# Performance work log

Hardware: AMD Instinct MI355X
Metric: run time of the kernel (lower is better)

Reference implementation:

```python
import jax, jax.numpy as jnp
import numpy as np

NEG_SLOPE_ATT = 0.2   # GATv2Conv attention leaky_relu slope
NEG_SLOPE_ACT = 0.01  # F.leaky_relu default between layers


def gatv2_layer(x, src, dst, edge_attr, Wl, Wr, We, att, concat):
    """PyG GATv2Conv (bias=False, residual=False, share_weights=False,
    add_self_loops=True with fill_value='mean' for edge_attr, eval mode)."""
    N = x.shape[0]
    H, C = att.shape
    E = src.shape[0]
    # self-loop edge attrs: mean of incoming edge attrs per node (fill_value='mean')
    deg = jax.ops.segment_sum(jnp.ones((E,), x.dtype), dst, num_segments=N)
    loop_attr = jax.ops.segment_sum(edge_attr, dst, num_segments=N) / jnp.maximum(deg, 1.0)[:, None]
    loop = jnp.arange(N)
    s = jnp.concatenate([src, loop])
    d = jnp.concatenate([dst, loop])
    ea = jnp.concatenate([edge_attr, loop_attr], axis=0)
    xl = (x @ Wl).reshape(N, H, C)  # lin_l -> source features (messages)
    xr = (x @ Wr).reshape(N, H, C)  # lin_r -> target features
    # edge-wise attention input: x_l[j] + x_r[i] + lin_edge(e_ij)  -> [E+N, H, C]
    e = xl[s] + xr[d] + (ea @ We).reshape(-1, H, C)
    e = jax.nn.leaky_relu(e, NEG_SLOPE_ATT)
    logits = jnp.einsum('ehc,hc->eh', e, att)  # [E+N, H]
    # numerically stable segment softmax over incoming edges per destination
    lmax = jax.ops.segment_max(logits, d, num_segments=N)  # every node has a self loop -> finite
    ex = jnp.exp(logits - lmax[d])
    denom = jax.ops.segment_sum(ex, d, num_segments=N)
    alpha = ex / (denom[d] + 1e-16)
    out = jax.ops.segment_sum(alpha[:, :, None] * xl[s], d, num_segments=N)  # [N, H, C]
    return out.reshape(N, H * C) if concat else out.mean(axis=1)


def setup_inputs() -> dict:
    key = jax.random.key(0)
    ks = jax.random.split(key, 12)
    N, E, F, H, C, EDIM, NCLS = 50000, 800000, 128, 4, 32, 16, 1
    HC = H * C  # 128
    sc = 0.1
    return {
        'x': jax.random.normal(ks[0], (N, F), jnp.float32),
        'edge_index': jax.random.randint(ks[1], (2, E), 0, N),
        'edge_attr': jax.random.normal(ks[2], (E, EDIM), jnp.float32),
        'Wl1': jax.random.normal(ks[3], (F, HC), jnp.float32) * sc,
        'Wr1': jax.random.normal(ks[4], (F, HC), jnp.float32) * sc,
        'We1': jax.random.normal(ks[5], (EDIM, HC), jnp.float32) * sc,
        'att1': jax.random.normal(ks[6], (H, C), jnp.float32) * sc,
        'Wl2': jax.random.normal(ks[7], (HC, H * NCLS), jnp.float32) * sc,
        'Wr2': jax.random.normal(ks[8], (HC, H * NCLS), jnp.float32) * sc,
        'We2': jax.random.normal(ks[9], (EDIM, H * NCLS), jnp.float32) * sc,
        'att2': jax.random.normal(ks[10], (H, NCLS), jnp.float32) * sc,
    }


def reference(x, edge_index, edge_attr, Wl1, Wr1, We1, att1, Wl2, Wr2, We2, att2):
    src, dst = edge_index[0], edge_index[1]
    h = gatv2_layer(x, src, dst, edge_attr, Wl1, Wr1, We1, att1, concat=True)
    h = jax.nn.leaky_relu(h, NEG_SLOPE_ACT)
    out = gatv2_layer(h, src, dst, edge_attr, Wl2, Wr2, We2, att2, concat=False)
    return out.reshape(-1)
```

## Files before the change

kernel.cpp:

```cpp
#include <hip/hip_runtime.h>
#include <math.h>


typedef __attribute__((ext_vector_type(8))) short bf16x8;
typedef __attribute__((ext_vector_type(4))) float f32x4;
typedef __attribute__((ext_vector_type(2))) float f32x2;
typedef _Float16 f16;
typedef __attribute__((ext_vector_type(2))) _Float16 f16x2;
typedef __attribute__((ext_vector_type(8))) _Float16 f16x8;

static __device__ __forceinline__ ushort f2bf(float f) {
    unsigned u = __float_as_uint(f);
    unsigned r = (u + 0x7fffu + ((u >> 16) & 1u)) >> 16;
    return (ushort)r;
}

static __device__ __forceinline__ float row_sum16(float x) {
    x += __int_as_float(__builtin_amdgcn_update_dpp(0, __float_as_int(x), 0x121, 0xf, 0xf, true));
    x += __int_as_float(__builtin_amdgcn_update_dpp(0, __float_as_int(x), 0x122, 0xf, 0xf, true));
    x += __int_as_float(__builtin_amdgcn_update_dpp(0, __float_as_int(x), 0x124, 0xf, 0xf, true));
    x += __int_as_float(__builtin_amdgcn_update_dpp(0, __float_as_int(x), 0x128, 0xf, 0xf, true));
    return x;
}

static __device__ __forceinline__ float red64(float x) {
    x = row_sum16(x);
    x += __shfl_xor(x, 16);
    x += __shfl_xor(x, 32);
    return x;
}

__global__ void k_count_deg(const int* __restrict__ dst, int* __restrict__ deg,
                            int* __restrict__ rank, int E) {
    int i = blockIdx.x * blockDim.x + threadIdx.x;
    if (i < E) rank[i] = atomicAdd(&deg[dst[i]], 1);
}

__global__ __launch_bounds__(1024) void k_scan1(const int* __restrict__ deg,
                                                int* __restrict__ rowptr,
                                                int* __restrict__ part, int N) {
    __shared__ int wsum[16];
    int t = threadIdx.x, l = t & 63, w = t >> 6;
    int i = blockIdx.x * 1024 + t;
    int v = (i < N) ? deg[i] : 0;
    int sc = v;
    #pragma unroll
    for (int off = 1; off < 64; off <<= 1) {
        int y = __shfl_up(sc, off);
        if (l >= off) sc += y;
    }
    if (l == 63) wsum[w] = sc;
    __syncthreads();
    if (w == 0) {
        int pv = (l < 16) ? wsum[l] : 0;
        int psc = pv;
        #pragma unroll
        for (int off = 1; off < 16; off <<= 1) {
            int y = __shfl_up(psc, off);
            if (l >= off) psc += y;
        }
        if (l < 16) wsum[l] = psc - pv;
    }
    __syncthreads();
    if (i < N) rowptr[i] = wsum[w] + sc - v;
    if (t == 1023) part[blockIdx.x] = wsum[15] + sc;
}

__global__ void k_scan2(int* __restrict__ part, int nb) {
    int l = threadIdx.x & 63;
    int run = 0;
    for (int base = 0; base < nb; base += 64) {
        int i = base + l;
        int v = (i < nb) ? part[i] : 0;
        int sc = v;
        #pragma unroll
        for (int off = 1; off < 64; off <<= 1) {
            int y = __shfl_up(sc, off);
            if (l >= off) sc += y;
        }
        if (i < nb) part[i] = run + sc - v;
        run += __shfl(sc, 63);
    }
}

__global__ void k_scan3(int* __restrict__ rowptr, const int* __restrict__ part, int N, int E) {
    int i = blockIdx.x * 256 + threadIdx.x;
    if (i < N) rowptr[i] += part[i >> 10];
    if (i == 0) rowptr[N] = E;
}

__global__ __launch_bounds__(256) void k_scatter_e(
    const int* __restrict__ dst, const int* __restrict__ src,
    const float* __restrict__ ea, const float* __restrict__ We2,
    const int* __restrict__ rowptr, const int* __restrict__ rank,
    f16* __restrict__ ea_f16, float* __restrict__ qe2,
    int* __restrict__ src_perm, int E) {
    __shared__ float sW[64];
    int t = threadIdx.x;
    if (t < 64) sW[t] = We2[t];
    __syncthreads();
    int i = blockIdx.x * 256 + t;
    if (i >= E) return;
    int d = dst[i];
    int pos = rowptr[d] + rank[i];
    src_perm[pos] = src[i];
    const float4* s4 = (const float4*)(ea + (size_t)i * 16);
    float4 r0 = s4[0], r1 = s4[1], r2 = s4[2], r3 = s4[3];
    f16x8 h0, h1;
    h0[0] = (f16)r0.x; h0[1] = (f16)r0.y; h0[2] = (f16)r0.z; h0[3] = (f16)r0.w;
    h0[4] = (f16)r1.x; h0[5] = (f16)r1.y; h0[6] = (f16)r1.z; h0[7] = (f16)r1.w;
    h1[0] = (f16)r2.x; h1[1] = (f16)r2.y; h1[2] = (f16)r2.z; h1[3] = (f16)r2.w;
    h1[4] = (f16)r3.x; h1[5] = (f16)r3.y; h1[6] = (f16)r3.z; h1[7] = (f16)r3.w;
    *(f16x8*)(ea_f16 + (size_t)pos * 16) = h0;
    *(f16x8*)(ea_f16 + (size_t)pos * 16 + 8) = h1;
    float a[16] = {r0.x, r0.y, r0.z, r0.w, r1.x, r1.y, r1.z, r1.w,
                   r2.x, r2.y, r2.z, r2.w, r3.x, r3.y, r3.z, r3.w};
    float q0 = 0.f, q1 = 0.f, q2v = 0.f, q3 = 0.f;
    #pragma unroll
    for (int k = 0; k < 16; ++k) {
        q0 += a[k] * sW[k * 4 + 0];
        q1 += a[k] * sW[k * 4 + 1];
        q2v += a[k] * sW[k * 4 + 2];
        q3 += a[k] * sW[k * 4 + 3];
    }
    *(float4*)(qe2 + (size_t)pos * 4) = make_float4(q0, q1, q2v, q3);
}

__global__ void k_wcvt(const float* __restrict__ Wl, const float* __restrict__ Wr,
                       const float* __restrict__ We1,
                       ushort* __restrict__ wcat_t, f16* __restrict__ we1h) {
    int i = blockIdx.x * 256 + threadIdx.x;
    if (i < 16 * 128) we1h[i] = (f16)We1[i];
    if (i >= 128 * 256) return;
    int n = i >> 7, k = i & 127;
    float v = (n < 128) ? Wl[k * 128 + n] : Wr[k * 128 + (n - 128)];
    wcat_t[i] = f2bf(v);
}

__global__ __launch_bounds__(256) void k_gemm1_mfma(
    const float* __restrict__ x, const ushort* __restrict__ wcat_t,
    ushort* __restrict__ xl, float* __restrict__ xr, int N) {
    __shared__ ushort xs[64 * 128];
    int t = threadIdx.x, l = t & 63, w = t >> 6;
    int r0 = blockIdx.x * 64;
    bf16x8 bf[4][4];
    {
        int coln = w * 64 + (l & 15);
        int kr = (l >> 4) * 8;
        #pragma unroll
        for (int nt = 0; nt < 4; ++nt)
            #pragma unroll
            for (int ks = 0; ks < 4; ++ks)
                bf[nt][ks] = *(const bf16x8*)&wcat_t[(size_t)(nt * 16 + coln) * 128 + ks * 32 + kr];
    }
    #pragma unroll
    for (int it = 0; it < 4; ++it) {
        int slot = t + 256 * it;
        int row = slot >> 4, ch = slot & 15;
        int grow = r0 + row;
        float v0 = 0.f, v1 = 0.f, v2 = 0.f, v3 = 0.f, v4 = 0.f, v5 = 0.f, v6 = 0.f, v7 = 0.f;
        if (grow < N) {
            float4 a = *(const float4*)(x + (size_t)grow * 128 + ch * 8);
            float4 b = *(const float4*)(x + (size_t)grow * 128 + ch * 8 + 4);
            v0 = a.x; v1 = a.y; v2 = a.z; v3 = a.w;
            v4 = b.x; v5 = b.y; v6 = b.z; v7 = b.w;
        }
        bf16x8 tv;
        tv[0] = (short)f2bf(v0); tv[1] = (short)f2bf(v1);
        tv[2] = (short)f2bf(v2); tv[3] = (short)f2bf(v3);
        tv[4] = (short)f2bf(v4); tv[5] = (short)f2bf(v5);
        tv[6] = (short)f2bf(v6); tv[7] = (short)f2bf(v7);
        int ch2 = ch ^ (row & 15);
        *(bf16x8*)&xs[row * 128 + ch2 * 8] = tv;
    }
    __syncthreads();
    f32x4 acc[4][4];
    #pragma unroll
    for (int mt = 0; mt < 4; ++mt)
        #pragma unroll
        for (int nt = 0; nt < 4; ++nt)
            acc[mt][nt] = (f32x4){0.f, 0.f, 0.f, 0.f};
    #pragma unroll
    for (int ks = 0; ks < 4; ++ks) {
        bf16x8 af[4];
        #pragma unroll
        for (int mt = 0; mt < 4; ++mt) {
            int row = mt * 16 + (l & 15);
            int ch = (ks * 4 + (l >> 4)) ^ (row & 15);
            af[mt] = *(const bf16x8*)&xs[row * 128 + ch * 8];
        }
        #pragma unroll
        for (int mt = 0; mt < 4; ++mt)
            #pragma unroll
            for (int nt = 0; nt < 4; ++nt)
                acc[mt][nt] = __builtin_amdgcn_mfma_f32_16x16x32_bf16(
                    af[mt], bf[nt][ks], acc[mt][nt], 0, 0, 0);
    }
    #pragma unroll
    for (int mt = 0; mt < 4; ++mt) {
        #pragma unroll
        for (int nt = 0; nt < 4; ++nt) {
            int colg = w * 64 + nt * 16 + (l & 15);
            #pragma unroll
            for (int r = 0; r < 4; ++r) {
                int rowg = r0 + mt * 16 + (l >> 4) * 4 + r;
                if (rowg < N) {
                    float val = acc[mt][nt][r];
                    if (colg < 128) xl[(size_t)rowg * 128 + colg] = f2bf(val);
                    else            xr[(size_t)rowg * 128 + (colg - 128)] = val;
                }
            }
        }
    }
}

__global__ __launch_bounds__(256, 4) void k_fused1_dot(
    const int* __restrict__ rowptr, const int* __restrict__ src_perm,
    const ushort* __restrict__ xl_bf, const float* __restrict__ xr,
    const f16* __restrict__ ea_f16, const f16* __restrict__ we1h,
    const float* __restrict__ att,
    const float* __restrict__ Wl2, const float* __restrict__ Wr2,
    float* __restrict__ xl2, float* __restrict__ xr2, int N) {
    int t = threadIdx.x, l = t & 63;
    int n = (blockIdx.x * 256 + t) >> 6;
    if (n >= N) return;
    const float RLN2 = 1.44269504f;
    const unsigned* xlw = (const unsigned*)xl_bf;
    f16x2 weX[8], weY[8];
    #pragma unroll
    for (int kp = 0; kp < 8; ++kp) {
        weX[kp][0] = we1h[(2 * kp) * 128 + 2 * l];
        weX[kp][1] = we1h[(2 * kp + 1) * 128 + 2 * l];
        weY[kp][0] = we1h[(2 * kp) * 128 + 2 * l + 1];
        weY[kp][1] = we1h[(2 * kp + 1) * 128 + 2 * l + 1];
    }
    f32x2 av = *(const f32x2*)(att + 2 * l);
    av = av * RLN2;
    f32x2 xrv = *(const f32x2*)(xr + (size_t)n * 128 + 2 * l);
    int rs = rowptr[n], re = rowptr[n + 1];
    int deg = re - rs;
    int urs = __builtin_amdgcn_readfirstlane(rs);
    f32x2 acc = {0.f, 0.f}, mq = {0.f, 0.f};
    float den = 0.f;
    #pragma unroll 2
    for (int slot = 0; slot < deg; ++slot) {
        unsigned jj = (unsigned)(urs + slot);
        const f16x2* ap = (const f16x2*)(ea_f16 + (size_t)jj * 16);
        int s = src_perm[jj];
        unsigned xw = xlw[(unsigned)s * 64u + (unsigned)l];
        float qx = 0.f, qy = 0.f;
        #pragma unroll
        for (int kp = 0; kp < 8; ++kp) {
            f16x2 a = ap[kp];
            qx = __builtin_amdgcn_fdot2(a, weX[kp], qx, false);
            qy = __builtin_amdgcn_fdot2(a, weY[kp], qy, false);
        }
        f32x2 q = {qx, qy};
        f32x2 xlv;
        xlv.x = __uint_as_float(xw << 16);
        xlv.y = __uint_as_float(xw & 0xffff0000u);
        f32x2 v = xrv + q + xlv;
        f32x2 u = __builtin_elementwise_max(v, 0.2f * v);
        f32x2 pt = av * u;
        float p = row_sum16(pt.x + pt.y);
        float w = exp2f(p);
        acc += xlv * w;
        den += w;
        mq += q;
    }
    {
        float inv = 1.f / (float)(deg > 1 ? deg : 1);
        f32x2 q = mq * inv;
        unsigned xw = xlw[(unsigned)n * 64u + (unsigned)l];
        f32x2 xlv;
        xlv.x = __uint_as_float(xw << 16);
        xlv.y = __uint_as_float(xw & 0xffff0000u);
        f32x2 v = xrv + q + xlv;
        f32x2 u = __builtin_elementwise_max(v, 0.2f * v);
        f32x2 pt = av * u;
        float p = row_sum16(pt.x + pt.y);
        float w = exp2f(p);
        acc += xlv * w;
        den += w;
    }
    float rdn = 1.f / (den + 1e-16f);
    float h0 = acc.x * rdn, h1 = acc.y * rdn;
    h0 = h0 > 0.f ? h0 : 0.01f * h0;
    h1 = h1 > 0.f ? h1 : 0.01f * h1;
    float4 wla = *(const float4*)(Wl2 + (size_t)(2 * l) * 4);
    float4 wlb = *(const float4*)(Wl2 + (size_t)(2 * l + 1) * 4);
    float4 wra = *(const float4*)(Wr2 + (size_t)(2 * l) * 4);
    float4 wrb = *(const float4*)(Wr2 + (size_t)(2 * l + 1) * 4);
    float q0 = red64(h0 * wla.x + h1 * wlb.x);
    float q1 = red64(h0 * wla.y + h1 * wlb.y);
    float q2 = red64(h0 * wla.z + h1 * wlb.z);
    float q3 = red64(h0 * wla.w + h1 * wlb.w);
    float q4 = red64(h0 * wra.x + h1 * wrb.x);
    float q5 = red64(h0 * wra.y + h1 * wrb.y);
    float q6 = red64(h0 * wra.z + h1 * wrb.z);
    float q7 = red64(h0 * wra.w + h1 * wrb.w);
    if (l == 0) {
        *(float4*)(xl2 + (size_t)n * 4) = make_float4(q0, q1, q2, q3);
        *(float4*)(xr2 + (size_t)n * 4) = make_float4(q4, q5, q6, q7);
    }
}

__global__ __launch_bounds__(256, 4) void k_fused2_q(
    const int* __restrict__ rowptr, const int* __restrict__ src_perm,
    const float* __restrict__ xl2, const float* __restrict__ xr2,
    const float* __restrict__ qe2, const float* __restrict__ att2,
    float* __restrict__ out, int N) {
    int t = threadIdx.x, l = t & 63, g = l & 15;
    int node = (((blockIdx.x * 256 + t) >> 6) << 2) + (l >> 4);
    if (node >= N) return;
    int rs = rowptr[node], re = rowptr[node + 1];
    int deg = re - rs;
    float4 xrv = *(const float4*)(xr2 + (size_t)node * 4);
    const float RLN2 = 1.44269504f;
    float a0 = att2[0] * RLN2, a1 = att2[1] * RLN2;
    float a2 = att2[2] * RLN2, a3 = att2[3] * RLN2;
    float ac0 = 0.f, ac1 = 0.f, ac2 = 0.f, ac3 = 0.f;
    float dn0 = 0.f, dn1 = 0.f, dn2 = 0.f, dn3 = 0.f;
    float mq0 = 0.f, mq1 = 0.f, mq2 = 0.f, mq3 = 0.f;
    for (int slot = g; slot < deg; slot += 16) {
        int row = rs + slot;
        int s = src_perm[row];
        float4 q = *(const float4*)(qe2 + (size_t)row * 4);
        float4 xv = *(const float4*)(xl2 + (size_t)s * 4);
        float v0 = xv.x + xrv.x + q.x; v0 = fmaxf(v0, 0.2f * v0);
        float v1 = xv.y + xrv.y + q.y; v1 = fmaxf(v1, 0.2f * v1);
        float v2 = xv.z + xrv.z + q.z; v2 = fmaxf(v2, 0.2f * v2);
        float v3 = xv.w + xrv.w + q.w; v3 = fmaxf(v3, 0.2f * v3);
        float w0 = exp2f(v0 * a0); ac0 += w0 * xv.x; dn0 += w0;
        float w1 = exp2f(v1 * a1); ac1 += w1 * xv.y; dn1 += w1;
        float w2 = exp2f(v2 * a2); ac2 += w2 * xv.z; dn2 += w2;
        float w3 = exp2f(v3 * a3); ac3 += w3 * xv.w; dn3 += w3;
        mq0 += q.x; mq1 += q.y; mq2 += q.z; mq3 += q.w;
    }
    ac0 = row_sum16(ac0); ac1 = row_sum16(ac1);
    ac2 = row_sum16(ac2); ac3 = row_sum16(ac3);
    dn0 = row_sum16(dn0); dn1 = row_sum16(dn1);
    dn2 = row_sum16(dn2); dn3 = row_sum16(dn3);
    mq0 = row_sum16(mq0); mq1 = row_sum16(mq1);
    mq2 = row_sum16(mq2); mq3 = row_sum16(mq3);
    {
        float inv = 1.f / (float)(deg > 1 ? deg : 1);
        float4 xv = *(const float4*)(xl2 + (size_t)node * 4);
        float v0 = xv.x + xrv.x + mq0 * inv; v0 = fmaxf(v0, 0.2f * v0);
        float v1 = xv.y + xrv.y + mq1 * inv; v1 = fmaxf(v1, 0.2f * v1);
        float v2 = xv.z + xrv.z + mq2 * inv; v2 = fmaxf(v2, 0.2f * v2);
        float v3 = xv.w + xrv.w + mq3 * inv; v3 = fmaxf(v3, 0.2f * v3);
        float w0 = exp2f(v0 * a0); ac0 += w0 * xv.x; dn0 += w0;
        float w1 = exp2f(v1 * a1); ac1 += w1 * xv.y; dn1 += w1;
        float w2 = exp2f(v2 * a2); ac2 += w2 * xv.z; dn2 += w2;
        float w3 = exp2f(v3 * a3); ac3 += w3 * xv.w; dn3 += w3;
    }
    if (g == 0) {
        float r = ac0 / (dn0 + 1e-16f) + ac1 / (dn1 + 1e-16f)
                + ac2 / (dn2 + 1e-16f) + ac3 / (dn3 + 1e-16f);
        out[node] = r * 0.25f;
    }
}

extern "C" void kernel_launch(void* const* d_in, const int* in_sizes, int n_in,
                              void* d_out, int out_size, void* d_ws, size_t ws_size,
                              hipStream_t stream) {
    const float* x         = (const float*)d_in[0];
    const int*   edge_index= (const int*)d_in[1];
    const float* edge_attr = (const float*)d_in[2];
    const float* Wl1       = (const float*)d_in[3];
    const float* Wr1       = (const float*)d_in[4];
    const float* We1       = (const float*)d_in[5];
    const float* att1      = (const float*)d_in[6];
    const float* Wl2       = (const float*)d_in[7];
    const float* Wr2       = (const float*)d_in[8];
    const float* We2       = (const float*)d_in[9];
    const float* att2      = (const float*)d_in[10];
    float* outp = (float*)d_out;

    const int F = 128, HC = 128;
    int N = in_sizes[0] / F;
    int E = in_sizes[1] / 2;
    const int* src = edge_index;
    const int* dst = edge_index + E;

    char* ws = (char*)d_ws;
    size_t off = 0;
    auto alloc = [&](size_t bytes) {
        char* p = ws + off;
        off += (bytes + 255) & ~(size_t)255;
        return p;
    };
    int*      deg      = (int*)alloc((size_t)N * 4);
    int*      rowptr   = (int*)alloc((size_t)(N + 1) * 4);
    int*      part     = (int*)alloc(((size_t)N / 1024 + 2) * 4);
    int*      rank     = (int*)alloc((size_t)E * 4);
    ushort*   wcat_t   = (ushort*)alloc((size_t)128 * 256 * 2);
    f16*      we1h     = (f16*)alloc((size_t)16 * 128 * 2);
    ushort*   xl_bf    = (ushort*)alloc((size_t)N * HC * 2);
    float*    xr1      = (float*)alloc((size_t)N * HC * 4);
    float*    xl2      = (float*)alloc((size_t)N * 4 * 4);
    float*    xr2      = (float*)alloc((size_t)N * 4 * 4);
    int*      src_perm = (int*)alloc((size_t)E * 4);
    float*    qe2      = (float*)alloc((size_t)E * 4 * 4);
    f16*      ea_f16   = (f16*)alloc((size_t)E * 16 * 2);

    int eb = (E + 255) / 256;
    int nb = (N + 1023) / 1024;

    hipMemsetAsync(deg, 0, (size_t)N * 4, stream);
    k_count_deg<<<eb, 256, 0, stream>>>(dst, deg, rank, E);
    k_scan1<<<nb, 1024, 0, stream>>>(deg, rowptr, part, N);
    k_scan2<<<1, 64, 0, stream>>>(part, nb);
    k_scan3<<<(N + 255) / 256, 256, 0, stream>>>(rowptr, part, N, E);
    k_scatter_e<<<eb, 256, 0, stream>>>(dst, src, edge_attr, We2, rowptr, rank,
                                        ea_f16, qe2, src_perm, E);
    k_wcvt<<<128, 256, 0, stream>>>(Wl1, Wr1, We1, wcat_t, we1h);
    k_gemm1_mfma<<<(N + 63) / 64, 256, 0, stream>>>(x, wcat_t, xl_bf, xr1, N);
    k_fused1_dot<<<(N + 3) / 4, 256, 0, stream>>>(rowptr, src_perm, xl_bf, xr1, ea_f16,
                                                  we1h, att1, Wl2, Wr2, xl2, xr2, N);
    k_fused2_q<<<(N + 15) / 16, 256, 0, stream>>>(rowptr, src_perm, xl2, xr2, qe2,
                                                  att2, outp, N);
}
```

Baseline: 214.6 us.

## Split wavefront into two half-waves processing two edges per iteration with prefetch

The layer-1 fused aggregation kernel now has each 64-lane wavefront handle two edges at once, with each 32-lane half owning 4 channels per lane. The head reduction shrinks to 8 lanes via DPP, and the two halves are combined with a cross-half shuffle at the end. The next edge's src index and xl row are software-prefetched, which aims to cut the serial per-edge latency chain of the gather loop. The cost is more registers (32 f16x2 weight registers, and the launch_bounds occupancy hint is removed) and masked wasted work when the degree is odd.

```diff
diff --git a/kernel.cpp b/kernel.cpp
--- a/kernel.cpp
+++ b/kernel.cpp
@@ -23,10 +23,10 @@
     return x;
 }
 
-static __device__ __forceinline__ float red64(float x) {
-    x = row_sum16(x);
-    x += __shfl_xor(x, 16);
-    x += __shfl_xor(x, 32);
+static __device__ __forceinline__ float sum8(float x) {
+    x += __int_as_float(__builtin_amdgcn_update_dpp(0, __float_as_int(x), 0xB1, 0xf, 0xf, true));
+    x += __int_as_float(__builtin_amdgcn_update_dpp(0, __float_as_int(x), 0x4E, 0xf, 0xf, true));
+    x += __int_as_float(__builtin_amdgcn_update_dpp(0, __float_as_int(x), 0x141, 0xf, 0xf, true));
     return x;
 }
 
@@ -214,7 +214,7 @@
     }
 }
 
-__global__ __launch_bounds__(256, 4) void k_fused1_dot(
+__global__ __launch_bounds__(256) void k_fused1_hw(
     const int* __restrict__ rowptr, const int* __restrict__ src_perm,
     const ushort* __restrict__ xl_bf, const float* __restrict__ xr,
     const f16* __restrict__ ea_f16, const f16* __restrict__ we1h,
@@ -222,83 +222,138 @@
     const float* __restrict__ Wl2, const float* __restrict__ Wr2,
     float* __restrict__ xl2, float* __restrict__ xr2, int N) {
     int t = threadIdx.x, l = t & 63;
+    int j = l & 31, half = l >> 5;
     int n = (blockIdx.x * 256 + t) >> 6;
     if (n >= N) return;
     const float RLN2 = 1.44269504f;
     const unsigned* xlw = (const unsigned*)xl_bf;
-    f16x2 weX[8], weY[8];
-    #pragma unroll
-    for (int kp = 0; kp < 8; ++kp) {
-        weX[kp][0] = we1h[(2 * kp) * 128 + 2 * l];
-        weX[kp][1] = we1h[(2 * kp + 1) * 128 + 2 * l];
-        weY[kp][0] = we1h[(2 * kp) * 128 + 2 * l + 1];
-        weY[kp][1] = we1h[(2 * kp + 1) * 128 + 2 * l + 1];
-    }
-    f32x2 av = *(const f32x2*)(att + 2 * l);
-    av = av * RLN2;
-    f32x2 xrv = *(const f32x2*)(xr + (size_t)n * 128 + 2 * l);
+    f16x2 w16[4][8];
+    #pragma unroll
+    for (int c = 0; c < 4; ++c)
+        #pragma unroll
+        for (int kp = 0; kp < 8; ++kp) {
+            w16[c][kp][0] = we1h[(2 * kp) * 128 + 4 * j + c];
+            w16[c][kp][1] = we1h[(2 * kp + 1) * 128 + 4 * j + c];
+        }
+    float4 av = *(const float4*)(att + 4 * j);
+    av.x *= RLN2; av.y *= RLN2; av.z *= RLN2; av.w *= RLN2;
+    float4 xrv = *(const float4*)(xr + (size_t)n * 128 + 4 * j);
     int rs = rowptr[n], re = rowptr[n + 1];
     int deg = re - rs;
     int urs = __builtin_amdgcn_readfirstlane(rs);
-    f32x2 acc = {0.f, 0.f}, mq = {0.f, 0.f};
+    float acc0 = 0.f, acc1 = 0.f, acc2 = 0.f, acc3 = 0.f;
+    float mq0 = 0.f, mq1 = 0.f, mq2 = 0.f, mq3 = 0.f;
     float den = 0.f;
-    #pragma unroll 2
-    for (int slot = 0; slot < deg; ++slot) {
-        unsigned jj = (unsigned)(urs + slot);
+    int niter = (deg + 1) >> 1;
+    float mk_nxt = 0.f;
+    unsigned jj_nxt = 0;
+    uint2 xw_nxt = make_uint2(0u, 0u);
+    if (niter > 0) {
+        int sA = half;
+        mk_nxt = (sA < deg) ? 1.f : 0.f;
+        int sc = (sA < deg) ? sA : (deg - 1);
+        jj_nxt = (unsigned)(urs + sc);
+        int s0 = src_perm[jj_nxt];
+        xw_nxt = *(const uint2*)(xlw + (size_t)(unsigned)s0 * 64u + 2u * j);
+    }
+    for (int it = 0; it < niter; ++it) {
+        float mk = mk_nxt;
+        unsigned jj = jj_nxt;
+        uint2 xw = xw_nxt;
+        if (it + 1 < niter) {
+            int sA = 2 * (it + 1) + half;
+            mk_nxt = (sA < deg) ? 1.f : 0.f;
+            int sc = (sA < deg) ? sA : (deg - 1);
+            jj_nxt = (unsigned)(urs + sc);
+            int s1 = src_perm[jj_nxt];
+            xw_nxt = *(const uint2*)(xlw + (size_t)(unsigned)s1 * 64u + 2u * j);
+        }
         const f16x2* ap = (const f16x2*)(ea_f16 + (size_t)jj * 16);
-        int s = src_perm[jj];
-        unsigned xw = xlw[(unsigned)s * 64u + (unsigned)l];
-        float qx = 0.f, qy = 0.f;
+        float q0 = 0.f, q1 = 0.f, q2 = 0.f, q3 = 0.f;
         #pragma unroll
         for (int kp = 0; kp < 8; ++kp) {
             f16x2 a = ap[kp];
-            qx = __builtin_amdgcn_fdot2(a, weX[kp], qx, false);
-            qy = __builtin_amdgcn_fdot2(a, weY[kp], qy, false);
-        }
-        f32x2 q = {qx, qy};
-        f32x2 xlv;
-        xlv.x = __uint_as_float(xw << 16);
-        xlv.y = __uint_as_float(xw & 0xffff0000u);
-        f32x2 v = xrv + q + xlv;
-        f32x2 u = __builtin_elementwise_max(v, 0.2f * v);
-        f32x2 pt = av * u;
-        float p = row_sum16(pt.x + pt.y);
-        float w = exp2f(p);
-        acc += xlv * w;
+            q0 = __builtin_amdgcn_fdot2(a, w16[0][kp], q0, false);
+            q1 = __builtin_amdgcn_fdot2(a, w16[1][kp], q1, false);
+            q2 = __builtin_amdgcn_fdot2(a, w16[2][kp], q2, false);
+            q3 = __builtin_amdgcn_fdot2(a, w16[3][kp], q3, false);
+        }
+        float x0 = __uint_as_float(xw.x << 16);
+        float x1 = __uint_as_float(xw.x & 0xffff0000u);
+        float x2 = __uint_as_float(xw.y << 16);
+        float x3 = __uint_as_float(xw.y & 0xffff0000u);
+        float v0 = xrv.x + q0 + x0;
+        float v1 = xrv.y + q1 + x1;
+        float v2 = xrv.z + q2 + x2;
+        float v3 = xrv.w + q3 + x3;
+        v0 = fmaxf(v0, 0.2f * v0);
+        v1 = fmaxf(v1, 0.2f * v1);
+        v2 = fmaxf(v2, 0.2f * v2);
+        v3 = fmaxf(v3, 0.2f * v3);
+        float p = av.x * v0 + av.y * v1 + av.z * v2 + av.w * v3;
+        p = sum8(p);
+        float w = exp2f(p) * mk;
+        acc0 += w * x0; acc1 += w * x1; acc2 += w * x2; acc3 += w * x3;
         den += w;
-        mq += q;
-    }
+        mq0 += mk * q0; mq1 += mk * q1; mq2 += mk * q2; mq3 += mk * q3;
+    }
+    acc0 += __shfl_xor(acc0, 32); acc1 += __shfl_xor(acc1, 32);
+    acc2 += __shfl_xor(acc2, 32); acc3 += __shfl_xor(acc3, 32);
+    mq0 += __shfl_xor(mq0, 32); mq1 += __shfl_xor(mq1, 32);
+    mq2 += __shfl_xor(mq2, 32); mq3 += __shfl_xor(mq3, 32);
+    den += __shfl_xor(den, 32);
     {
         float inv = 1.f / (float)(deg > 1 ? deg : 1);
-        f32x2 q = mq * inv;
-        unsigned xw = xlw[(unsigned)n * 64u + (unsigned)l];
-        f32x2 xlv;
-        xlv.x = __uint_as_float(xw << 16);
-        xlv.y = __uint_as_float(xw & 0xffff0000u);
-        f32x2 v = xrv + q + xlv;
-        f32x2 u = __builtin_elementwise_max(v, 0.2f * v);
-        f32x2 pt = av * u;
-        float p = row_sum16(pt.x + pt.y);
+        float q0 = mq0 * inv, q1 = mq1 * inv, q2 = mq2 * inv, q3 = mq3 * inv;
+        uint2 xw = *(const uint2*)(xlw + (size_t)(unsigned)n * 64u + 2u * j);
+        float x0 = __uint_as_float(xw.x << 16);
+        float x1 = __uint_as_float(xw.x & 0xffff0000u);
+        float x2 = __uint_as_float(xw.y << 16);
+        float x3 = __uint_as_float(xw.y & 0xffff0000u);
+        float v0 = xrv.x + q0 + x0;
+        float v1 = xrv.y + q1 + x1;
+        float v2 = xrv.z + q2 + x2;
+        float v3 = xrv.w + q3 + x3;
+        v0 = fmaxf(v0, 0.2f * v0);
+        v1 = fmaxf(v1, 0.2f * v1);
+        v2 = fmaxf(v2, 0.2f * v2);
+        v3 = fmaxf(v3, 0.2f * v3);
+        float p = av.x * v0 + av.y * v1 + av.z * v2 + av.w * v3;
+        p = sum8(p);
         float w = exp2f(p);
-        acc += xlv * w;
+        acc0 += w * x0; acc1 += w * x1; acc2 += w * x2; acc3 += w * x3;
         den += w;
     }
     float rdn = 1.f / (den + 1e-16f);
-    float h0 = acc.x * rdn, h1 = acc.y * rdn;
+    float h0 = acc0 * rdn, h1 = acc1 * rdn, h2 = acc2 * rdn, h3 = acc3 * rdn;
     h0 = h0 > 0.f ? h0 : 0.01f * h0;
     h1 = h1 > 0.f ? h1 : 0.01f * h1;
-    float4 wla = *(const float4*)(Wl2 + (size_t)(2 * l) * 4);
-    float4 wlb = *(const float4*)(Wl2 + (size_t)(2 * l + 1) * 4);
-    float4 wra = *(const float4*)(Wr2 + (size_t)(2 * l) * 4);
-    float4 wrb = *(const float4*)(Wr2 + (size_t)(2 * l + 1) * 4);
-    float q0 = red64(h0 * wla.x + h1 * wlb.x);
-    float q1 = red64(h0 * wla.y + h1 * wlb.y);
-    float q2 = red64(h0 * wla.z + h1 * wlb.z);
-    float q3 = red64(h0 * wla.w + h1 * wlb.w);
-    float q4 = red64(h0 * wra.x + h1 * wrb.x);
-    float q5 = red64(h0 * wra.y + h1 * wrb.y);
-    float q6 = red64(h0 * wra.z + h1 * wrb.z);
-    float q7 = red64(h0 * wra.w + h1 * wrb.w);
+    h2 = h2 > 0.f ? h2 : 0.01f * h2;
+    h3 = h3 > 0.f ? h3 : 0.01f * h3;
+    float4 wl0 = *(const float4*)(Wl2 + (size_t)(4 * j + 0) * 4);
+    float4 wl1 = *(const float4*)(Wl2 + (size_t)(4 * j + 1) * 4);
+    float4 wl2v = *(const float4*)(Wl2 + (size_t)(4 * j + 2) * 4);
+    float4 wl3 = *(const float4*)(Wl2 + (size_t)(4 * j + 3) * 4);
+    float4 wr0 = *(const float4*)(Wr2 + (size_t)(4 * j + 0) * 4);
+    float4 wr1 = *(const float4*)(Wr2 + (size_t)(4 * j + 1) * 4);
+    float4 wr2v = *(const float4*)(Wr2 + (size_t)(4 * j + 2) * 4);
+    float4 wr3 = *(const float4*)(Wr2 + (size_t)(4 * j + 3) * 4);
+    float q0 = h0 * wl0.x + h1 * wl1.x + h2 * wl2v.x + h3 * wl3.x;
+    float q1 = h0 * wl0.y + h1 * wl1.y + h2 * wl2v.y + h3 * wl3.y;
+    float q2 = h0 * wl0.z + h1 * wl1.z + h2 * wl2v.z + h3 * wl3.z;
+    float q3 = h0 * wl0.w + h1 * wl1.w + h2 * wl2v.w + h3 * wl3.w;
+    float q4 = h0 * wr0.x + h1 * wr1.x + h2 * wr2v.x + h3 * wr3.x;
+    float q5 = h0 * wr0.y + h1 * wr1.y + h2 * wr2v.y + h3 * wr3.y;
+    float q6 = h0 * wr0.z + h1 * wr1.z + h2 * wr2v.z + h3 * wr3.z;
+    float q7 = h0 * wr0.w + h1 * wr1.w + h2 * wr2v.w + h3 * wr3.w;
+    q0 = row_sum16(q0); q0 += __shfl_xor(q0, 16);
+    q1 = row_sum16(q1); q1 += __shfl_xor(q1, 16);
+    q2 = row_sum16(q2); q2 += __shfl_xor(q2, 16);
+    q3 = row_sum16(q3); q3 += __shfl_xor(q3, 16);
+    q4 = row_sum16(q4); q4 += __shfl_xor(q4, 16);
+    q5 = row_sum16(q5); q5 += __shfl_xor(q5, 16);
+    q6 = row_sum16(q6); q6 += __shfl_xor(q6, 16);
+    q7 = row_sum16(q7); q7 += __shfl_xor(q7, 16);
     if (l == 0) {
         *(float4*)(xl2 + (size_t)n * 4) = make_float4(q0, q1, q2, q3);
         *(float4*)(xr2 + (size_t)n * 4) = make_float4(q4, q5, q6, q7);
@@ -417,8 +472,8 @@
                                         ea_f16, qe2, src_perm, E);
     k_wcvt<<<128, 256, 0, stream>>>(Wl1, Wr1, We1, wcat_t, we1h);
     k_gemm1_mfma<<<(N + 63) / 64, 256, 0, stream>>>(x, wcat_t, xl_bf, xr1, N);
-    k_fused1_dot<<<(N + 3) / 4, 256, 0, stream>>>(rowptr, src_perm, xl_bf, xr1, ea_f16,
-                                                  we1h, att1, Wl2, Wr2, xl2, xr2, N);
+    k_fused1_hw<<<(N + 3) / 4, 256, 0, stream>>>(rowptr, src_perm, xl_bf, xr1, ea_f16,
+                                                 we1h, att1, Wl2, Wr2, xl2, xr2, N);
     k_fused2_q<<<(N + 15) / 16, 256, 0, stream>>>(rowptr, src_perm, xl2, xr2, qe2,
                                                   att2, outp, N);
 }
```

After: 249.1 us. +16.1%, slower.
